# Performance work log

Hardware: AMD Instinct MI355X
Metric: run time of the kernel (lower is better)

Reference implementation:

```python
import jax, jax.numpy as jnp
import numpy as np

N = 100000
E = 1600000
D_IN = 128
D_HID = 128
EDGE_DIM = 1
K_NBR = 16


def _lin_params(key, fan_in, fan_out):
    k1, k2 = jax.random.split(key)
    s = 1.0 / np.sqrt(fan_in)
    W = jax.random.uniform(k1, (fan_in, fan_out), jnp.float32, -s, s)
    b = jax.random.uniform(k2, (fan_out,), jnp.float32, -s, s)
    return W, b


def setup_inputs() -> dict:
    key = jax.random.key(0)
    ks = jax.random.split(key, 16)
    x = jax.random.normal(ks[0], (N, D_IN), jnp.float32)
    edge_index = jax.random.randint(ks[1], (2, E), 0, N, jnp.int64 if jax.config.jax_enable_x64 else jnp.int32)
    neighbor_indices = jax.random.randint(ks[2], (K_NBR,), 0, N, jnp.int32)
    edge_attr = jax.random.normal(ks[3], (E, EDGE_DIM), jnp.float32)
    # conv1: edge lin (edge_dim -> in), mlp (in -> hid -> hid)
    We1, be1 = _lin_params(ks[4], EDGE_DIM, D_IN)
    W11, b11 = _lin_params(ks[5], D_IN, D_HID)
    W12, b12 = _lin_params(ks[6], D_HID, D_HID)
    # conv2: edge lin (edge_dim -> hid), mlp (hid -> hid -> hid)
    We2, be2 = _lin_params(ks[7], EDGE_DIM, D_HID)
    W21, b21 = _lin_params(ks[8], D_HID, D_HID)
    W22, b22 = _lin_params(ks[9], D_HID, D_HID)
    # policy head
    Wl1, bl1 = _lin_params(ks[10], 3 * D_HID, D_HID)
    Wl2, bl2 = _lin_params(ks[11], D_HID, 1)
    return {
        "x": x, "edge_index": edge_index, "curr_idx": 0, "dest_idx": 99999,
        "neighbor_indices": neighbor_indices, "edge_attr": edge_attr,
        "We1": We1, "be1": be1, "W11": W11, "b11": b11, "W12": W12, "b12": b12,
        "We2": We2, "be2": be2, "W21": W21, "b21": b21, "W22": W22, "b22": b22,
        "Wl1": Wl1, "bl1": bl1, "Wl2": Wl2, "bl2": bl2,
    }


def _gine_conv(x, src, dst, edge_attr, We, be, W1, b1, W2, b2, eps=0.0):
    # PyG GINEConv: message = relu(x_j + lin(edge_attr)), sum-aggregate at target,
    # out = mlp((1+eps)*x + aggr)
    e = edge_attr @ We + be                      # [E, d]
    m = jax.nn.relu(x[src] + e)                  # [E, d] gather + fused add/relu
    aggr = jax.ops.segment_sum(m, dst, num_segments=x.shape[0])  # [N, d]
    h = (1.0 + eps) * x + aggr
    return jax.nn.relu(h @ W1 + b1) @ W2 + b2


def reference(x, edge_index, curr_idx, dest_idx, neighbor_indices, edge_attr,
              We1, be1, W11, b11, W12, b12,
              We2, be2, W21, b21, W22, b22,
              Wl1, bl1, Wl2, bl2):
    src, dst = edge_index[0], edge_index[1]
    # encoder (eval mode: dropout is identity)
    h = _gine_conv(x, src, dst, edge_attr, We1, be1, W11, b11, W12, b12)
    h = jax.nn.relu(h)
    node_embs = _gine_conv(h, src, dst, edge_attr, We2, be2, W21, b21, W22, b22)
    # policy head: batched over neighbors instead of python loop
    curr = node_embs[curr_idx]                   # [d]
    dest = node_embs[dest_idx]                   # [d]
    nbr = node_embs[neighbor_indices]            # [K, d]
    Kn = nbr.shape[0]
    cat = jnp.concatenate(
        [jnp.broadcast_to(curr, (Kn, curr.shape[0])),
         jnp.broadcast_to(dest, (Kn, dest.shape[0])),
         nbr], axis=-1)                          # [K, 3d]
    q = jax.nn.relu(cat @ Wl1 + bl1) @ Wl2 + bl2  # [K, 1]
    return q[:, 0]                               # [K]
```

## Files before the change

kernel.cpp:

```cpp
#include <hip/hip_runtime.h>

constexpr int Nn   = 100000;
constexpr int Ee   = 1600000;
constexpr int D    = 128;
constexpr int NT   = 18;

constexpr int CAPS = 1024;
constexpr int CAP2 = 1024;

constexpr int BMW  = 3136;
constexpr int LOCT = 64;
constexpr int LOCS = 128;
constexpr int MAXM = 96;

#define HDR_CNTS  1
#define HDR_CNTL2 3

constexpr size_t OFF_HDR   = 0;
constexpr size_t OFF_BMS   = 256;
constexpr size_t OFF_A1    = 12800;
constexpr size_t ZERO_BYTES= 537088;
constexpr size_t OFF_MARKS = 537088;
constexpr size_t OFF_SLIST = 937088;
constexpr size_t OFF_L2    = 941184;
constexpr size_t OFF_HS    = 953472;
constexpr size_t OFF_EMB   = 1477760;
constexpr size_t WS_NEED   = 1486976;

__global__ void k_zero(float4* p, int n4) {
    int i = blockIdx.x * blockDim.x + threadIdx.x;
    int stride = gridDim.x * blockDim.x;
    for (; i < n4; i += stride) p[i] = float4{0.f, 0.f, 0.f, 0.f};
}

__device__ __forceinline__ void claim_node(int v, int* markS, int* hdr,
                                           int* Slist, unsigned* bmS) {
    unsigned bit = 1u << (v & 31);
    unsigned old = atomicOr(&bmS[(unsigned)v >> 5], bit);
    if (!(old & bit)) {
        int s = atomicAdd(&hdr[HDR_CNTS], 1);
        if (s < CAPS) { Slist[s] = v; markS[v] = 2 + s; }
    }
}

__global__ void __launch_bounds__(256)
k_scanT(const int* __restrict__ src, const int* __restrict__ dst,
        const int* __restrict__ cur, const int* __restrict__ des,
        const int* __restrict__ nbr,
        int* __restrict__ hdr, int* __restrict__ markS,
        unsigned* __restrict__ bmS, int* __restrict__ Slist,
        int* __restrict__ L2) {
    __shared__ unsigned bm[BMW];
    __shared__ int sT[NT];
    __shared__ int loc[LOCT * 3];
    __shared__ int lcnt, lbase;
    int t = threadIdx.x;
    if (t == 0) lcnt = 0;
    for (int w = t; w < BMW / 4; w += 256)
        reinterpret_cast<uint4*>(bm)[w] = uint4{0u, 0u, 0u, 0u};
    if (t < NT) sT[t] = (t == 0) ? cur[0] : (t == 1) ? des[0] : nbr[t - 2];
    __syncthreads();
    if (t < NT) {
        int v = sT[t];
        atomicOr(&bm[(unsigned)v >> 5], 1u << (v & 31));
        if (blockIdx.x == 0) claim_node(v, markS, hdr, Slist, bmS);
    }
    __syncthreads();
    int stride = gridDim.x * blockDim.x;
    for (int q = blockIdx.x * blockDim.x + t; q < Ee / 4; q += stride) {
        int4 d4 = reinterpret_cast<const int4*>(dst)[q];
        int dsv[4] = {d4.x, d4.y, d4.z, d4.w};
        #pragma unroll
        for (int j = 0; j < 4; ++j) {
            int d = dsv[j];
            if ((bm[(unsigned)d >> 5] >> (d & 31)) & 1u) {
                int slot = 0;
                while (sT[slot] != d) ++slot;
                int e = q * 4 + j;
                int s = src[e];
                claim_node(s, markS, hdr, Slist, bmS);
                int li = atomicAdd(&lcnt, 1);
                if (li < LOCT) {
                    loc[3*li] = s; loc[3*li+1] = e; loc[3*li+2] = slot;
                } else {
                    int idx = atomicAdd(&hdr[HDR_CNTL2], 1);
                    if (idx < CAP2) { L2[3*idx] = s; L2[3*idx+1] = e; L2[3*idx+2] = slot; }
                }
            }
        }
    }
    __syncthreads();
    if (t == 0) {
        int n = lcnt < LOCT ? lcnt : LOCT;
        lcnt = n;
        if (n) lbase = atomicAdd(&hdr[HDR_CNTL2], n);
    }
    __syncthreads();
    for (int i = t; i < lcnt; i += 256) {
        int idx = lbase + i;
        if (idx < CAP2) {
            L2[3*idx] = loc[3*i]; L2[3*idx+1] = loc[3*i+1]; L2[3*idx+2] = loc[3*i+2];
        }
    }
}

__global__ void __launch_bounds__(256)
k_scanSA(const float* __restrict__ x, const int* __restrict__ src,
         const int* __restrict__ dst, const float* __restrict__ ea,
         const float* __restrict__ We1, const float* __restrict__ be1,
         const int* __restrict__ markS, const unsigned* __restrict__ bmS,
         float* __restrict__ A1) {
    __shared__ unsigned bm[BMW];
    __shared__ int loc[LOCS * 3];
    __shared__ int lcnt;
    int t = threadIdx.x;
    if (t == 0) lcnt = 0;
    const uint4* g4 = reinterpret_cast<const uint4*>(bmS);
    for (int w = t; w < BMW / 4; w += 256) reinterpret_cast<uint4*>(bm)[w] = g4[w];
    __syncthreads();
    int stride = gridDim.x * blockDim.x;
    for (int q = blockIdx.x * blockDim.x + t; q < Ee / 4; q += stride) {
        int4 d4 = reinterpret_cast<const int4*>(dst)[q];
        int dsv[4] = {d4.x, d4.y, d4.z, d4.w};
        #pragma unroll
        for (int j = 0; j < 4; ++j) {
            int d = dsv[j];
            if ((bm[(unsigned)d >> 5] >> (d & 31)) & 1u) {
                int v = markS[d];
                if (v >= 2 && (unsigned)(v - 2) < (unsigned)CAPS) {
                    int e = q * 4 + j;
                    int li = atomicAdd(&lcnt, 1);
                    if (li < LOCS) {
                        loc[3*li] = src[e]; loc[3*li+1] = e; loc[3*li+2] = v - 2;
                    } else {
                        float a = ea[e];
                        int s = src[e];
                        for (int d0 = 0; d0 < D; ++d0)
                            atomicAdd(&A1[(size_t)(v - 2) * D + d0],
                                      fmaxf(fmaf(a, We1[d0], be1[d0]) + x[(size_t)s * D + d0], 0.f));
                    }
                }
            }
        }
    }
    __syncthreads();
    int n = lcnt < LOCS ? lcnt : LOCS;
    int w = t >> 6, l = t & 63;
    int d0 = l * 2;
    for (int i = w; i < n; i += 4) {
        int s = loc[3*i], e = loc[3*i+1], slot = loc[3*i+2];
        float a = ea[e];
        float2 xv = *reinterpret_cast<const float2*>(&x[(size_t)s * D + d0]);
        float2 wv = *reinterpret_cast<const float2*>(&We1[d0]);
        float2 bv = *reinterpret_cast<const float2*>(&be1[d0]);
        atomicAdd(&A1[(size_t)slot * D + d0],     fmaxf(fmaf(a, wv.x, bv.x) + xv.x, 0.f));
        atomicAdd(&A1[(size_t)slot * D + d0 + 1], fmaxf(fmaf(a, wv.y, bv.y) + xv.y, 0.f));
    }
}

__global__ void __launch_bounds__(256)
k_mlpS(const float* __restrict__ x, const float* __restrict__ A,
       const int* __restrict__ Slist, const int* __restrict__ hdr,
       const float* __restrict__ W1, const float* __restrict__ b1,
       const float* __restrict__ W2, const float* __restrict__ b2,
       float* __restrict__ Hs) {
    __shared__ float buf[D];
    __shared__ float hid[D];
    __shared__ float part[2][D];
    int cnt = hdr[HDR_CNTS];
    if (cnt > CAPS) cnt = CAPS;
    int tid = threadIdx.x;
    int t = tid & 127, g = tid >> 7;
    for (int b = blockIdx.x; b < cnt; b += gridDim.x) {
        if (g == 0) {
            int node = Slist[b];
            buf[t] = x[(size_t)node * D + t] + A[(size_t)b * D + t];
        }
        __syncthreads();
        float acc = 0.f;
        int c0 = g * 64;
        #pragma unroll 8
        for (int c = c0; c < c0 + 64; ++c) acc = fmaf(buf[c], W1[c * D + t], acc);
        part[g][t] = acc;
        __syncthreads();
        if (g == 0) hid[t] = fmaxf(part[0][t] + part[1][t] + b1[t], 0.f);
        __syncthreads();
        acc = 0.f;
        #pragma unroll 8
        for (int c = c0; c < c0 + 64; ++c) acc = fmaf(hid[c], W2[c * D + t], acc);
        part[g][t] = acc;
        __syncthreads();
        if (g == 0) Hs[(size_t)b * D + t] = fmaxf(part[0][t] + part[1][t] + b2[t], 0.f);
        __syncthreads();
    }
}

__global__ void __launch_bounds__(512)
k_tailT(const float* __restrict__ Hs, const int* __restrict__ L2,
        const int* __restrict__ hdr, const int* __restrict__ markS,
        const int* __restrict__ cur, const int* __restrict__ des,
        const int* __restrict__ nbr, const float* __restrict__ ea,
        const float* __restrict__ We2, const float* __restrict__ be2,
        const float* __restrict__ W21, const float* __restrict__ b21,
        const float* __restrict__ W22, const float* __restrict__ b22,
        float* __restrict__ EMB) {
    __shared__ int sT[NT];
    __shared__ float buf[D];
    __shared__ float hid[D];
    __shared__ float part[4][D];
    __shared__ int mss[MAXM];
    __shared__ float mea[MAXM];
    __shared__ int mcnt;
    int tid = threadIdx.x;
    int b = blockIdx.x;
    if (tid == 0) mcnt = 0;
    if (tid < NT) sT[tid] = (tid == 0) ? cur[0] : (tid == 1) ? des[0] : nbr[tid - 2];
    __syncthreads();
    int node = sT[b];
    for (int j = 0; j < b; ++j) if (sT[j] == node) return;
    int cnt2 = hdr[HDR_CNTL2]; if (cnt2 > CAP2) cnt2 = CAP2;
    for (int i = tid; i < cnt2; i += 512) {
        if (L2[3*i + 2] == b) {
            int li = atomicAdd(&mcnt, 1);
            if (li < MAXM) {
                mss[li] = markS[L2[3*i]] - 2;
                mea[li] = ea[L2[3*i + 1]];
            }
        }
    }
    __syncthreads();
    int n = mcnt < MAXM ? mcnt : MAXM;
    int t = tid & 127, g = tid >> 7;
    float w2 = We2[t], bb2 = be2[t];
    float a = 0.f;
    for (int i = g; i < n; i += 4) {
        int ss = mss[i];
        if ((unsigned)ss < (unsigned)CAPS)
            a += fmaxf(fmaf(mea[i], w2, bb2) + Hs[(size_t)ss * D + t], 0.f);
    }
    part[g][t] = a;
    __syncthreads();
    if (g == 0) {
        int sst = markS[node] - 2;
        float self = ((unsigned)sst < (unsigned)CAPS) ? Hs[(size_t)sst * D + t] : 0.f;
        buf[t] = self + part[0][t] + part[1][t] + part[2][t] + part[3][t];
    }
    __syncthreads();
    float acc = 0.f;
    int c0 = g * 32;
    #pragma unroll 8
    for (int c = c0; c < c0 + 32; ++c) acc = fmaf(buf[c], W21[c * D + t], acc);
    part[g][t] = acc;
    __syncthreads();
    if (g == 0) hid[t] = fmaxf(part[0][t] + part[1][t] + part[2][t] + part[3][t] + b21[t], 0.f);
    __syncthreads();
    acc = 0.f;
    #pragma unroll 8
    for (int c = c0; c < c0 + 32; ++c) acc = fmaf(hid[c], W22[c * D + t], acc);
    part[g][t] = acc;
    __syncthreads();
    if (g == 0)
        EMB[b * D + t] = part[0][t] + part[1][t] + part[2][t] + part[3][t] + b22[t];
}

__global__ void __launch_bounds__(512)
k_policy(const float* __restrict__ EMB,
         const int* __restrict__ cur, const int* __restrict__ des,
         const int* __restrict__ nbr,
         const float* __restrict__ Wl1, const float* __restrict__ bl1,
         const float* __restrict__ Wl2, const float* __restrict__ bl2,
         float* __restrict__ out) {
    __shared__ int sT[NT];
    __shared__ float cat[3 * D];
    __shared__ float part[4][D];
    __shared__ float red[D];
    int tid = threadIdx.x;
    int k = blockIdx.x;
    if (tid < NT) sT[tid] = (tid == 0) ? cur[0] : (tid == 1) ? des[0] : nbr[tid - 2];
    __syncthreads();
    int dsl = (sT[1] == sT[0]) ? 0 : 1;
    int nn = sT[2 + k];
    int nsl = 2 + k;
    for (int j = 0; j < 2 + k; ++j) if (sT[j] == nn) { nsl = j; break; }
    if (tid < 3 * D) {
        int seg = tid >> 7;
        int t = tid & (D - 1);
        int slot = (seg == 0) ? 0 : (seg == 1) ? dsl : nsl;
        cat[tid] = EMB[slot * D + t];
    }
    __syncthreads();
    int h = tid >> 7;
    int t = tid & (D - 1);
    float acc = 0.f;
    int c0 = h * 96;
    #pragma unroll 8
    for (int c = c0; c < c0 + 96; ++c)
        acc = fmaf(cat[c], Wl1[c * D + t], acc);
    part[h][t] = acc;
    __syncthreads();
    if (tid < D) {
        float v = part[0][t] + part[1][t] + part[2][t] + part[3][t] + bl1[t];
        red[t] = fmaxf(v, 0.f) * Wl2[t];
    }
    __syncthreads();
    for (int s = 64; s > 0; s >>= 1) {
        if (tid < s) red[tid] += red[tid + s];
        __syncthreads();
    }
    if (tid == 0) out[k] = red[0] + bl2[0];
}

extern "C" void kernel_launch(void* const* d_in, const int* in_sizes, int n_in,
                              void* d_out, int out_size, void* d_ws, size_t ws_size,
                              hipStream_t stream) {
    if (ws_size < WS_NEED) return;

    const float* x   = (const float*)d_in[0];
    const int*   ei  = (const int*)d_in[1];
    const int*   cur = (const int*)d_in[2];
    const int*   des = (const int*)d_in[3];
    const int*   nbr = (const int*)d_in[4];
    const float* ea  = (const float*)d_in[5];
    const float* We1 = (const float*)d_in[6];
    const float* be1 = (const float*)d_in[7];
    const float* W11 = (const float*)d_in[8];
    const float* b11 = (const float*)d_in[9];
    const float* W12 = (const float*)d_in[10];
    const float* b12 = (const float*)d_in[11];
    const float* We2 = (const float*)d_in[12];
    const float* be2 = (const float*)d_in[13];
    const float* W21 = (const float*)d_in[14];
    const float* b21 = (const float*)d_in[15];
    const float* W22 = (const float*)d_in[16];
    const float* b22 = (const float*)d_in[17];
    const float* Wl1 = (const float*)d_in[18];
    const float* bl1 = (const float*)d_in[19];
    const float* Wl2 = (const float*)d_in[20];
    const float* bl2 = (const float*)d_in[21];
    float* out = (float*)d_out;

    char*     ws    = (char*)d_ws;
    int*      hdr   = (int*)(ws + OFF_HDR);
    unsigned* bmS   = (unsigned*)(ws + OFF_BMS);
    float*    A1    = (float*)(ws + OFF_A1);
    int*      markS = (int*)(ws + OFF_MARKS);
    int*      Slist = (int*)(ws + OFF_SLIST);
    int*      L2    = (int*)(ws + OFF_L2);
    float*    Hs    = (float*)(ws + OFF_HS);
    float*    EMB   = (float*)(ws + OFF_EMB);

    const int* srcp = ei;
    const int* dstp = ei + Ee;

    k_zero  <<<132, 256, 0, stream>>>((float4*)ws, (int)(ZERO_BYTES / 16));
    k_scanT <<<512, 256, 0, stream>>>(srcp, dstp, cur, des, nbr,
                                      hdr, markS, bmS, Slist, L2);
    k_scanSA<<<512, 256, 0, stream>>>(x, srcp, dstp, ea, We1, be1,
                                      markS, bmS, A1);
    k_mlpS  <<<320, 256, 0, stream>>>(x, A1, Slist, hdr, W11, b11, W12, b12, Hs);
    k_tailT <<<NT, 512, 0, stream>>>(Hs, L2, hdr, markS, cur, des, nbr, ea,
                                     We2, be2, W21, b21, W22, b22, EMB);
    k_policy<<<16, 512, 0, stream>>>(EMB, cur, des, nbr, Wl1, bl1, Wl2, bl2, out);
}
```

Before: 47.91 us.

## Fuse second GINE layer tail with policy head and fold zeroing into scan

The separate zeroing kernel is replaced. The small header and bitmap region is cleared with hipMemsetAsync, and the A1 accumulator is zeroed inside the first scan kernel. The per-target tail kernel and the policy kernel are merged into one kernel with one block per neighbour. Each block recomputes the conv2 embeddings for curr, dest and its own neighbour, then runs the policy MLP directly. This removes a launch and the intermediate EMB buffer round trip. The cost is redundant recomputation of the curr and dest embeddings in every block, plus longer serial work per block.

```diff
diff --git a/kernel.cpp b/kernel.cpp
--- a/kernel.cpp
+++ b/kernel.cpp
@@ -18,20 +18,13 @@
 
 constexpr size_t OFF_HDR   = 0;
 constexpr size_t OFF_BMS   = 256;
+constexpr size_t MEMSET_B  = 12800;
 constexpr size_t OFF_A1    = 12800;
-constexpr size_t ZERO_BYTES= 537088;
 constexpr size_t OFF_MARKS = 537088;
 constexpr size_t OFF_SLIST = 937088;
 constexpr size_t OFF_L2    = 941184;
 constexpr size_t OFF_HS    = 953472;
-constexpr size_t OFF_EMB   = 1477760;
-constexpr size_t WS_NEED   = 1486976;
-
-__global__ void k_zero(float4* p, int n4) {
-    int i = blockIdx.x * blockDim.x + threadIdx.x;
-    int stride = gridDim.x * blockDim.x;
-    for (; i < n4; i += stride) p[i] = float4{0.f, 0.f, 0.f, 0.f};
-}
+constexpr size_t WS_NEED   = 1477760;
 
 __device__ __forceinline__ void claim_node(int v, int* markS, int* hdr,
                                            int* Slist, unsigned* bmS) {
@@ -49,12 +42,15 @@
         const int* __restrict__ nbr,
         int* __restrict__ hdr, int* __restrict__ markS,
         unsigned* __restrict__ bmS, int* __restrict__ Slist,
-        int* __restrict__ L2) {
+        int* __restrict__ L2, float4* __restrict__ A1z) {
     __shared__ unsigned bm[BMW];
     __shared__ int sT[NT];
     __shared__ int loc[LOCT * 3];
     __shared__ int lcnt, lbase;
     int t = threadIdx.x;
+    int gtid = blockIdx.x * blockDim.x + t;
+    int gstride = gridDim.x * blockDim.x;
+    for (int i = gtid; i < 32768; i += gstride) A1z[i] = float4{0.f, 0.f, 0.f, 0.f};
     if (t == 0) lcnt = 0;
     for (int w = t; w < BMW / 4; w += 256)
         reinterpret_cast<uint4*>(bm)[w] = uint4{0u, 0u, 0u, 0u};
@@ -66,8 +62,7 @@
         if (blockIdx.x == 0) claim_node(v, markS, hdr, Slist, bmS);
     }
     __syncthreads();
-    int stride = gridDim.x * blockDim.x;
-    for (int q = blockIdx.x * blockDim.x + t; q < Ee / 4; q += stride) {
+    for (int q = gtid; q < Ee / 4; q += gstride) {
         int4 d4 = reinterpret_cast<const int4*>(dst)[q];
         int dsv[4] = {d4.x, d4.y, d4.z, d4.w};
         #pragma unroll
@@ -196,118 +191,108 @@
 }
 
 __global__ void __launch_bounds__(512)
-k_tailT(const float* __restrict__ Hs, const int* __restrict__ L2,
+k_tail2(const float* __restrict__ Hs, const int* __restrict__ L2,
         const int* __restrict__ hdr, const int* __restrict__ markS,
         const int* __restrict__ cur, const int* __restrict__ des,
         const int* __restrict__ nbr, const float* __restrict__ ea,
         const float* __restrict__ We2, const float* __restrict__ be2,
         const float* __restrict__ W21, const float* __restrict__ b21,
         const float* __restrict__ W22, const float* __restrict__ b22,
-        float* __restrict__ EMB) {
+        const float* __restrict__ Wl1, const float* __restrict__ bl1,
+        const float* __restrict__ Wl2, const float* __restrict__ bl2,
+        float* __restrict__ out) {
     __shared__ int sT[NT];
-    __shared__ float buf[D];
-    __shared__ float hid[D];
-    __shared__ float part[4][D];
-    __shared__ int mss[MAXM];
-    __shared__ float mea[MAXM];
-    __shared__ int mcnt;
-    int tid = threadIdx.x;
-    int b = blockIdx.x;
-    if (tid == 0) mcnt = 0;
-    if (tid < NT) sT[tid] = (tid == 0) ? cur[0] : (tid == 1) ? des[0] : nbr[tid - 2];
-    __syncthreads();
-    int node = sT[b];
-    for (int j = 0; j < b; ++j) if (sT[j] == node) return;
-    int cnt2 = hdr[HDR_CNTL2]; if (cnt2 > CAP2) cnt2 = CAP2;
-    for (int i = tid; i < cnt2; i += 512) {
-        if (L2[3*i + 2] == b) {
-            int li = atomicAdd(&mcnt, 1);
-            if (li < MAXM) {
-                mss[li] = markS[L2[3*i]] - 2;
-                mea[li] = ea[L2[3*i + 1]];
-            }
-        }
-    }
-    __syncthreads();
-    int n = mcnt < MAXM ? mcnt : MAXM;
-    int t = tid & 127, g = tid >> 7;
-    float w2 = We2[t], bb2 = be2[t];
-    float a = 0.f;
-    for (int i = g; i < n; i += 4) {
-        int ss = mss[i];
-        if ((unsigned)ss < (unsigned)CAPS)
-            a += fmaxf(fmaf(mea[i], w2, bb2) + Hs[(size_t)ss * D + t], 0.f);
-    }
-    part[g][t] = a;
-    __syncthreads();
-    if (g == 0) {
-        int sst = markS[node] - 2;
-        float self = ((unsigned)sst < (unsigned)CAPS) ? Hs[(size_t)sst * D + t] : 0.f;
-        buf[t] = self + part[0][t] + part[1][t] + part[2][t] + part[3][t];
-    }
-    __syncthreads();
-    float acc = 0.f;
-    int c0 = g * 32;
-    #pragma unroll 8
-    for (int c = c0; c < c0 + 32; ++c) acc = fmaf(buf[c], W21[c * D + t], acc);
-    part[g][t] = acc;
-    __syncthreads();
-    if (g == 0) hid[t] = fmaxf(part[0][t] + part[1][t] + part[2][t] + part[3][t] + b21[t], 0.f);
-    __syncthreads();
-    acc = 0.f;
-    #pragma unroll 8
-    for (int c = c0; c < c0 + 32; ++c) acc = fmaf(hid[c], W22[c * D + t], acc);
-    part[g][t] = acc;
-    __syncthreads();
-    if (g == 0)
-        EMB[b * D + t] = part[0][t] + part[1][t] + part[2][t] + part[3][t] + b22[t];
-}
-
-__global__ void __launch_bounds__(512)
-k_policy(const float* __restrict__ EMB,
-         const int* __restrict__ cur, const int* __restrict__ des,
-         const int* __restrict__ nbr,
-         const float* __restrict__ Wl1, const float* __restrict__ bl1,
-         const float* __restrict__ Wl2, const float* __restrict__ bl2,
-         float* __restrict__ out) {
-    __shared__ int sT[NT];
-    __shared__ float cat[3 * D];
+    __shared__ float buf[3][D];
+    __shared__ float hid[3][D];
+    __shared__ float emb[3][D];
     __shared__ float part[4][D];
     __shared__ float red[D];
+    __shared__ int   mss[3][MAXM];
+    __shared__ float mea[3][MAXM];
+    __shared__ int   mcnt[3];
     int tid = threadIdx.x;
     int k = blockIdx.x;
     if (tid < NT) sT[tid] = (tid == 0) ? cur[0] : (tid == 1) ? des[0] : nbr[tid - 2];
+    if (tid < 3) mcnt[tid] = 0;
     __syncthreads();
     int dsl = (sT[1] == sT[0]) ? 0 : 1;
     int nn = sT[2 + k];
     int nsl = 2 + k;
     for (int j = 0; j < 2 + k; ++j) if (sT[j] == nn) { nsl = j; break; }
-    if (tid < 3 * D) {
-        int seg = tid >> 7;
-        int t = tid & (D - 1);
-        int slot = (seg == 0) ? 0 : (seg == 1) ? dsl : nsl;
-        cat[tid] = EMB[slot * D + t];
-    }
-    __syncthreads();
-    int h = tid >> 7;
-    int t = tid & (D - 1);
-    float acc = 0.f;
-    int c0 = h * 96;
-    #pragma unroll 8
-    for (int c = c0; c < c0 + 96; ++c)
-        acc = fmaf(cat[c], Wl1[c * D + t], acc);
-    part[h][t] = acc;
-    __syncthreads();
-    if (tid < D) {
-        float v = part[0][t] + part[1][t] + part[2][t] + part[3][t] + bl1[t];
-        red[t] = fmaxf(v, 0.f) * Wl2[t];
-    }
-    __syncthreads();
-    for (int s = 64; s > 0; s >>= 1) {
-        if (tid < s) red[tid] += red[tid + s];
-        __syncthreads();
-    }
-    if (tid == 0) out[k] = red[0] + bl2[0];
+    const int rs[3] = {0, dsl, nsl};
+    int cnt2 = hdr[HDR_CNTL2]; if (cnt2 > CAP2) cnt2 = CAP2;
+    for (int i = tid; i < cnt2; i += 512) {
+        int slot = L2[3*i + 2];
+        bool m0 = (slot == rs[0]), m1 = (slot == rs[1]), m2 = (slot == rs[2]);
+        if (m0 | m1 | m2) {
+            int sm = markS[L2[3*i]] - 2;
+            float av = ea[L2[3*i + 1]];
+            if (m0) { int li = atomicAdd(&mcnt[0], 1); if (li < MAXM) { mss[0][li] = sm; mea[0][li] = av; } }
+            if (m1) { int li = atomicAdd(&mcnt[1], 1); if (li < MAXM) { mss[1][li] = sm; mea[1][li] = av; } }
+            if (m2) { int li = atomicAdd(&mcnt[2], 1); if (li < MAXM) { mss[2][li] = sm; mea[2][li] = av; } }
+        }
+    }
+    __syncthreads();
+    int t = tid & 127, g = tid >> 7;
+    float w2 = We2[t], bb2 = be2[t];
+    #pragma unroll
+    for (int r = 0; r < 3; ++r) {
+        int n = mcnt[r] < MAXM ? mcnt[r] : MAXM;
+        float a = 0.f;
+        for (int i = g; i < n; i += 4) {
+            int ss = mss[r][i];
+            if ((unsigned)ss < (unsigned)CAPS)
+                a += fmaxf(fmaf(mea[r][i], w2, bb2) + Hs[(size_t)ss * D + t], 0.f);
+        }
+        part[g][t] = a;
+        __syncthreads();
+        if (g == 0) {
+            int sst = markS[sT[rs[r]]] - 2;
+            float self = ((unsigned)sst < (unsigned)CAPS) ? Hs[(size_t)sst * D + t] : 0.f;
+            buf[r][t] = self + part[0][t] + part[1][t] + part[2][t] + part[3][t];
+        }
+        __syncthreads();
+    }
+    int c0 = g * 32;
+    #pragma unroll
+    for (int r = 0; r < 3; ++r) {
+        float acc = 0.f;
+        #pragma unroll 8
+        for (int c = c0; c < c0 + 32; ++c) acc = fmaf(buf[r][c], W21[c * D + t], acc);
+        part[g][t] = acc;
+        __syncthreads();
+        if (g == 0) hid[r][t] = fmaxf(part[0][t] + part[1][t] + part[2][t] + part[3][t] + b21[t], 0.f);
+        __syncthreads();
+    }
+    #pragma unroll
+    for (int r = 0; r < 3; ++r) {
+        float acc = 0.f;
+        #pragma unroll 8
+        for (int c = c0; c < c0 + 32; ++c) acc = fmaf(hid[r][c], W22[c * D + t], acc);
+        part[g][t] = acc;
+        __syncthreads();
+        if (g == 0) emb[r][t] = part[0][t] + part[1][t] + part[2][t] + part[3][t] + b22[t];
+        __syncthreads();
+    }
+    {
+        float acc = 0.f;
+        int p0 = g * 96;
+        #pragma unroll 8
+        for (int c = p0; c < p0 + 96; ++c)
+            acc = fmaf(emb[c >> 7][c & 127], Wl1[c * D + t], acc);
+        part[g][t] = acc;
+        __syncthreads();
+        if (tid < D) {
+            float v = part[0][t] + part[1][t] + part[2][t] + part[3][t] + bl1[t];
+            red[t] = fmaxf(v, 0.f) * Wl2[t];
+        }
+        __syncthreads();
+        for (int s = 64; s > 0; s >>= 1) {
+            if (tid < s) red[tid] += red[tid + s];
+            __syncthreads();
+        }
+        if (tid == 0) out[k] = red[0] + bl2[0];
+    }
 }
 
 extern "C" void kernel_launch(void* const* d_in, const int* in_sizes, int n_in,
@@ -347,18 +332,17 @@
     int*      Slist = (int*)(ws + OFF_SLIST);
     int*      L2    = (int*)(ws + OFF_L2);
     float*    Hs    = (float*)(ws + OFF_HS);
-    float*    EMB   = (float*)(ws + OFF_EMB);
 
     const int* srcp = ei;
     const int* dstp = ei + Ee;
 
-    k_zero  <<<132, 256, 0, stream>>>((float4*)ws, (int)(ZERO_BYTES / 16));
+    hipMemsetAsync(ws, 0, MEMSET_B, stream);
     k_scanT <<<512, 256, 0, stream>>>(srcp, dstp, cur, des, nbr,
-                                      hdr, markS, bmS, Slist, L2);
+                                      hdr, markS, bmS, Slist, L2, (float4*)A1);
     k_scanSA<<<512, 256, 0, stream>>>(x, srcp, dstp, ea, We1, be1,
                                       markS, bmS, A1);
     k_mlpS  <<<320, 256, 0, stream>>>(x, A1, Slist, hdr, W11, b11, W12, b12, Hs);
-    k_tailT <<<NT, 512, 0, stream>>>(Hs, L2, hdr, markS, cur, des, nbr, ea,
-                                     We2, be2, W21, b21, W22, b22, EMB);
-    k_policy<<<16, 512, 0, stream>>>(EMB, cur, des, nbr, Wl1, bl1, Wl2, bl2, out);
-}
+    k_tail2 <<<16, 512, 0, stream>>>(Hs, L2, hdr, markS, cur, des, nbr, ea,
+                                     We2, be2, W21, b21, W22, b22,
+                                     Wl1, bl1, Wl2, bl2, out);
+}
```

After: 52.73 us. 10.1% more time.
